# Kernel optimization log

Measured on AMD Instinct MI355X. Metric: run time of the kernel, lower is better.

The kernel has to match this reference:

```python
import jax, jax.numpy as jnp
import numpy as np

TOP_K = 700
NUM_GROUPS = 4
OUT_H, OUT_W = 256, 256  # original image size (output_shape)


def setup_inputs() -> dict:
    key = jax.random.key(0)
    k1, k2, k3 = jax.random.split(key, 3)
    B, E, H, W = 2, 8, 64, 64
    return {
        "objectness_logits": jax.random.normal(k1, (B, 1, H, W), dtype=jnp.float32),
        "mask_encodings": jax.random.normal(k2, (B, E, H, W), dtype=jnp.float32),
        "weights": jax.random.normal(k3, (B, (E + 1) * NUM_GROUPS, H, W), dtype=jnp.float32),
    }


def reference(objectness_logits, mask_encodings, weights):
    B, E, H, W = mask_encodings.shape
    K = TOP_K
    # objectness = sigmoid(logits); top-k over flattened spatial positions
    obj = jax.nn.sigmoid(objectness_logits).reshape(B, -1)  # [B, H*W]
    scores, idx = jax.lax.top_k(obj, K)                      # [B, K] each
    # gather per-instance dynamic conv weights (batch_select2d equivalent)
    w = weights.transpose(0, 2, 3, 1).reshape(B, -1, (E + 1) * NUM_GROUPS)  # [B, H*W, 36]
    w_sel = jnp.take_along_axis(w, idx[:, :, None], axis=1)                  # [B, K, 36]
    w_sel = w_sel.reshape(B, K * NUM_GROUPS, E + 1)                          # [B, K*4, E+1]
    wmat = w_sel[..., :E]   # [B, K*4, E] conv 1x1 filters
    bias = w_sel[..., E]    # [B, K*4]
    # grouped 1x1 conv with groups=B == per-batch matmul over encoding channels
    m = jnp.einsum('bke,behw->bkhw', wmat, mask_encodings) + bias[:, :, None, None]
    m = jax.nn.sigmoid(m)
    # masks[:, i::4] product over the 4 groups per instance
    m = m.reshape(B, K, NUM_GROUPS, H, W).prod(axis=2)  # [B, K, H, W]
    # bilinear upsample to output shape (torch align_corners=False == jax half-pixel)
    m = jax.image.resize(m, (B, K, OUT_H, OUT_W), method='bilinear')
    return m, scores
```

## Files before the change

### kernel.cpp

```cpp
#include <hip/hip_runtime.h>
#include <cstdint>
#include <cstddef>

#define TOPK 700
#define NPIX 4096
#define NG 4
#define NE 8
#define NW 36

typedef float nt_float4 __attribute__((ext_vector_type(4)));

__global__ __launch_bounds__(256) void topk_kernel(
    const float* __restrict__ logits,
    int* __restrict__ sel_idx,
    float* __restrict__ scores_out) {
  __shared__ __attribute__((aligned(16))) unsigned long long keys[NPIX];

  const int b   = blockIdx.x >> 6;
  const int blk = blockIdx.x & 63;
  const float* src = logits + b * NPIX;

  for (int i = threadIdx.x; i < NPIX; i += 256) {
    float x = src[i];
    float s = 1.0f / (1.0f + expf(-x));
    keys[i] = (((unsigned long long)__float_as_uint(s)) << 12)
              | (unsigned long long)(4095 - i);
  }
  __syncthreads();

  const int e = blk * 64 + (threadIdx.x >> 2);
  const int q = threadIdx.x & 3;
  const unsigned long long mykey = keys[e];

  const ulonglong2* k2 = (const ulonglong2*)keys;
  int rank = 0;
  const int base = q * 512;
  #pragma unroll 8
  for (int jj = 0; jj < 512; ++jj) {
    ulonglong2 kk = k2[base + jj];
    rank += (kk.x > mykey);
    rank += (kk.y > mykey);
  }
  rank += __shfl_xor(rank, 1);
  rank += __shfl_xor(rank, 2);

  if (q == 0 && rank < TOPK) {
    int idx = 4095 - (int)(mykey & 0xFFFULL);
    sel_idx[b * TOPK + rank]    = idx;
    scores_out[b * TOPK + rank] = __uint_as_float((unsigned)(mykey >> 12));
  }
}

__global__ __launch_bounds__(256) void mask_kernel(
    const float* __restrict__ enc,
    const float* __restrict__ weights,
    const int* __restrict__ sel_idx,
    float* __restrict__ out_m) {
  __shared__ float ws[NW];
  __shared__ __attribute__((aligned(16))) float tile[18 * 64];

  const int blk = blockIdx.x;
  const int bk  = blk >> 2;
  const int qs  = blk & 3;
  const int b   = (bk >= TOPK) ? 1 : 0;
  const int tid = threadIdx.x;

  const int p = sel_idx[bk];
  if (tid < NW) ws[tid] = weights[(size_t)(b * NW + tid) * NPIX + p];
  __syncthreads();

  float wreg[NW];
  #pragma unroll
  for (int c = 0; c < NW; ++c) wreg[c] = ws[c];

  const int row0 = qs * 16 - 1;
  const float* eb = enc + (size_t)b * NE * NPIX;

  #pragma unroll
  for (int pass = 0; pass < 2; ++pass) {
    if (pass == 0 || tid < 32) {
      const int qq   = tid + pass * 256;
      const int j    = qq >> 4;
      const int col4 = (qq & 15) << 2;
      const int g    = row0 + j;
      const int gc   = (g < 0) ? 0 : ((g > 63) ? 63 : g);
      const int src4 = gc * 64 + col4;
      float4 ev[NE];
      #pragma unroll
      for (int ch = 0; ch < NE; ++ch)
        ev[ch] = *(const float4*)(eb + (size_t)ch * NPIX + src4);
      float4 s = make_float4(1.f, 1.f, 1.f, 1.f);
      #pragma unroll
      for (int g2 = 0; g2 < NG; ++g2) {
        float zx = wreg[g2 * 9 + 8], zy = zx, zz = zx, zw = zx;
        #pragma unroll
        for (int ch = 0; ch < NE; ++ch) {
          float w = wreg[g2 * 9 + ch];
          zx = fmaf(w, ev[ch].x, zx);
          zy = fmaf(w, ev[ch].y, zy);
          zz = fmaf(w, ev[ch].z, zz);
          zw = fmaf(w, ev[ch].w, zw);
        }
        s.x *= __builtin_amdgcn_rcpf(1.f + __expf(-zx));
        s.y *= __builtin_amdgcn_rcpf(1.f + __expf(-zy));
        s.z *= __builtin_amdgcn_rcpf(1.f + __expf(-zz));
        s.w *= __builtin_amdgcn_rcpf(1.f + __expf(-zw));
      }
      *(float4*)(&tile[j * 64 + col4]) = s;
    }
  }
  __syncthreads();

  const int tx = tid & 63;
  const int ty = tid >> 6;

  const int cxm = (tx > 0) ? tx - 1 : 0;
  const int cxp = (tx < 63) ? tx + 1 : 63;

  const float base_y = ty * 0.25f - 0.375f;
  const float fy0 = floorf(base_y);
  const float wy  = base_y - fy0;
  const int jbase = (ty < 2) ? 0 : 1;

  float* orow = out_m + (size_t)bk * 65536 + (size_t)(qs * 64 + ty) * 256 + 4 * tx;

  const float* r0 = &tile[jbase * 64];
  float am = r0[cxm], a0 = r0[tx], ap = r0[cxp];

  #pragma unroll 4
  for (int i = 0; i < 16; ++i) {
    const float* r1 = &tile[(jbase + i + 1) * 64];
    float bm = r1[cxm], b0 = r1[tx], bp = r1[cxp];
    float vm = fmaf(wy, bm - am, am);
    float v0 = fmaf(wy, b0 - a0, a0);
    float vp = fmaf(wy, bp - ap, ap);
    nt_float4 o;
    o.x = vm * 0.375f + v0 * 0.625f;
    o.y = vm * 0.125f + v0 * 0.875f;
    o.z = v0 * 0.875f + vp * 0.125f;
    o.w = v0 * 0.625f + vp * 0.375f;
    __builtin_nontemporal_store(o, (nt_float4*)(orow + (size_t)i * 1024));
    am = bm; a0 = b0; ap = bp;
  }
}

extern "C" void kernel_launch(void* const* d_in, const int* in_sizes, int n_in,
                              void* d_out, int out_size, void* d_ws, size_t ws_size,
                              hipStream_t stream) {
  const float* logits  = (const float*)d_in[0];
  const float* enc     = (const float*)d_in[1];
  const float* weights = (const float*)d_in[2];

  float* out        = (float*)d_out;
  float* out_m      = out;
  float* out_scores = out + (size_t)2 * TOPK * 256 * 256;
  int*   sel_idx    = (int*)d_ws;

  topk_kernel<<<128, 256, 0, stream>>>(logits, sel_idx, out_scores);
  mask_kernel<<<4 * 2 * TOPK, 256, 0, stream>>>(enc, weights, sel_idx, out_m);
}
```

Before: 394.6 us.

## Split mask computation and upsampling into separate kernels via workspace tiles

Replaces the fused mask kernel with two kernels: one computes each instance's full 64x64 sigmoid-product mask into a workspace buffer, and a grid-stride kernel then upsamples rows using wave shuffles for horizontal neighbours. This removes the recomputation of the halo rows that each quarter-block did in the fused version and gives more uniform write parallelism. In exchange it adds an extra global round trip of about 23 MB of intermediate tiles and one more launch. It falls back to the old fused path if the workspace is too small.

After: 404.6 us. +2.5%, slower.

```diff
diff --git a/kernel.cpp b/kernel.cpp
--- a/kernel.cpp
+++ b/kernel.cpp
@@ -48,6 +48,96 @@
     int idx = 4095 - (int)(mykey & 0xFFFULL);
     sel_idx[b * TOPK + rank]    = idx;
     scores_out[b * TOPK + rank] = __uint_as_float((unsigned)(mykey >> 12));
+  }
+}
+
+__global__ __launch_bounds__(256) void tile_kernel(
+    const float* __restrict__ enc,
+    const float* __restrict__ weights,
+    const int* __restrict__ sel_idx,
+    float* __restrict__ tiles) {
+  __shared__ float ws[NW];
+
+  const int bk  = blockIdx.x;
+  const int b   = (bk >= TOPK) ? 1 : 0;
+  const int tid = threadIdx.x;
+
+  const int p = sel_idx[bk];
+  if (tid < NW) ws[tid] = weights[(size_t)(b * NW + tid) * NPIX + p];
+  __syncthreads();
+
+  float wreg[NW];
+  #pragma unroll
+  for (int c = 0; c < NW; ++c) wreg[c] = ws[c];
+
+  const float* eb = enc + (size_t)b * NE * NPIX;
+  float* tb = tiles + (size_t)bk * NPIX;
+
+  #pragma unroll
+  for (int it = 0; it < 4; ++it) {
+    int p4 = (tid + 256 * it) * 4;
+    float4 ev[NE];
+    #pragma unroll
+    for (int ch = 0; ch < NE; ++ch)
+      ev[ch] = *(const float4*)(eb + (size_t)ch * NPIX + p4);
+    float4 s = make_float4(1.f, 1.f, 1.f, 1.f);
+    #pragma unroll
+    for (int g = 0; g < NG; ++g) {
+      float zx = wreg[g * 9 + 8], zy = zx, zz = zx, zw = zx;
+      #pragma unroll
+      for (int ch = 0; ch < NE; ++ch) {
+        float w = wreg[g * 9 + ch];
+        zx = fmaf(w, ev[ch].x, zx);
+        zy = fmaf(w, ev[ch].y, zy);
+        zz = fmaf(w, ev[ch].z, zz);
+        zw = fmaf(w, ev[ch].w, zw);
+      }
+      s.x *= __builtin_amdgcn_rcpf(1.f + __expf(-zx));
+      s.y *= __builtin_amdgcn_rcpf(1.f + __expf(-zy));
+      s.z *= __builtin_amdgcn_rcpf(1.f + __expf(-zz));
+      s.w *= __builtin_amdgcn_rcpf(1.f + __expf(-zw));
+    }
+    *(float4*)(tb + p4) = s;
+  }
+}
+
+__global__ __launch_bounds__(256) void upsample_kernel(
+    const float* __restrict__ tiles,
+    float* __restrict__ out_m) {
+  const int lane = threadIdx.x & 63;
+  const int wv   = threadIdx.x >> 6;
+  const int lm   = (lane > 0)  ? lane - 1 : 0;
+  const int lp   = (lane < 63) ? lane + 1 : 63;
+
+  const int nrows = 2 * TOPK * 256;
+  for (int r = blockIdx.x * 4 + wv; r < nrows; r += gridDim.x * 4) {
+    const int bk = r >> 8;
+    const int oy = r & 255;
+
+    const float in_y = oy * 0.25f - 0.375f;
+    const float fy0  = floorf(in_y);
+    const float wy   = in_y - fy0;
+    const int y0  = (int)fy0;
+    const int y0c = (y0 > 0) ? y0 : 0;
+    const int y1c = (y0 + 1 < 63) ? y0 + 1 : 63;
+
+    const float* t0 = tiles + (size_t)bk * NPIX + y0c * 64;
+    const float* t1 = tiles + (size_t)bk * NPIX + y1c * 64;
+    float a0 = t0[lane];
+    float b0 = t1[lane];
+    float am = __shfl(a0, lm, 64), ap = __shfl(a0, lp, 64);
+    float bm = __shfl(b0, lm, 64), bp = __shfl(b0, lp, 64);
+
+    float vm = fmaf(wy, bm - am, am);
+    float v0 = fmaf(wy, b0 - a0, a0);
+    float vp = fmaf(wy, bp - ap, ap);
+    nt_float4 o;
+    o.x = vm * 0.375f + v0 * 0.625f;
+    o.y = vm * 0.125f + v0 * 0.875f;
+    o.z = v0 * 0.875f + vp * 0.125f;
+    o.w = v0 * 0.625f + vp * 0.375f;
+    __builtin_nontemporal_store(
+        o, (nt_float4*)(out_m + (size_t)bk * 65536 + (size_t)oy * 256 + 4 * lane));
   }
 }
 
@@ -157,5 +247,14 @@
   int*   sel_idx    = (int*)d_ws;
 
   topk_kernel<<<128, 256, 0, stream>>>(logits, sel_idx, out_scores);
-  mask_kernel<<<4 * 2 * TOPK, 256, 0, stream>>>(enc, weights, sel_idx, out_m);
-}
+
+  const size_t tiles_off  = 8192;
+  const size_t tiles_need = tiles_off + (size_t)2 * TOPK * NPIX * sizeof(float);
+  if (ws_size >= tiles_need) {
+    float* tiles = (float*)((char*)d_ws + tiles_off);
+    tile_kernel<<<2 * TOPK, 256, 0, stream>>>(enc, weights, sel_idx, tiles);
+    upsample_kernel<<<2048, 256, 0, stream>>>(tiles, out_m);
+  } else {
+    mask_kernel<<<4 * 2 * TOPK, 256, 0, stream>>>(enc, weights, sel_idx, out_m);
+  }
+}
```
